# Kernel optimization log

Hardware: AMD Instinct MI355X
Metric: run time of the kernel (lower is better)

## Reference

```python
import jax, jax.numpy as jnp
import numpy as np

VOXEL_SIZE = np.array([0.1, 0.1, 0.1], np.float32)
PC_MIN = np.array([-70.4, -40.0, -3.0], np.float32)
STRIDE = 8
NZ, NY, NX = 5, 100, 176          # dense voxel grid dims at this stride (z, y, x)
G = 6                             # ROI grid size
C_IN, C_MID = 64, 32              # backbone channels, per-point MLP widths
N_ROIS, N_VOX = 256, 30000
FC = 256

_o = np.arange(-1, 2)
OFFSETS = np.stack(np.meshgrid(_o, _o, _o, indexing='ij'), -1).reshape(-1, 3).astype(np.int32)  # (27,3) (dx,dy,dz)


def setup_inputs() -> dict:
    rng = np.random.default_rng(0)
    # rois: [x, y, z, dx, dy, dz, heading]
    ctr = np.stack([rng.uniform(-60, 60, N_ROIS), rng.uniform(-35, 35, N_ROIS), rng.uniform(-2.0, 0.5, N_ROIS)], -1)
    size = np.stack([rng.uniform(3.0, 5.0, N_ROIS), rng.uniform(1.5, 2.2, N_ROIS), rng.uniform(1.3, 1.9, N_ROIS)], -1)
    yaw = rng.uniform(-np.pi, np.pi, (N_ROIS, 1))
    rois = np.concatenate([ctr, size, yaw], -1).astype(np.float32)
    # unique sparse voxel coords stored as (x, y, z)
    flat = rng.choice(NZ * NY * NX, N_VOX, replace=False)
    z, y, x = np.unravel_index(flat, (NZ, NY, NX))
    voxel_coords = np.stack([x, y, z], -1).astype(np.int32)

    def W(*s):
        return jnp.asarray((rng.standard_normal(s) / np.sqrt(s[-1])).astype(np.float32))

    pre = G ** 3 * C_MID  # 6912, channel-major flattened pooled features
    return dict(
        rois=jnp.asarray(rois),
        voxel_features=jnp.asarray(rng.standard_normal((N_VOX, C_IN)).astype(np.float32)),
        voxel_coords=jnp.asarray(voxel_coords),
        w_mlp1=W(C_IN, C_MID), w_mlp2=W(C_MID, C_MID),
        w_fc1=W(FC, pre), w_fc2=W(FC, FC),
        w_cls1=W(FC, FC), w_cls2=W(FC, FC), w_cls3=W(1, FC), b_cls3=jnp.zeros((1,), jnp.float32),
        w_iou1=W(FC, FC), w_iou2=W(FC, FC), w_iou3=W(1, FC), b_iou3=jnp.zeros((1,), jnp.float32),
        w_reg1=W(FC, FC), w_reg2=W(FC, FC), w_reg3=W(7, FC) * 0.001, b_reg3=jnp.zeros((7,), jnp.float32),
    )


def _grid_points(rois):
    # dense GxGxG grid in each roi local frame, rotated by heading, shifted to center
    idx = jnp.stack(jnp.meshgrid(*([jnp.arange(G)] * 3), indexing='ij'), -1).reshape(-1, 3).astype(jnp.float32)
    size = rois[:, 3:6]                                               # (N,3)
    local = (idx[None] + 0.5) / G * size[:, None] - size[:, None] * 0.5  # (N,216,3)
    c, s = jnp.cos(rois[:, 6])[:, None], jnp.sin(rois[:, 6])[:, None]
    gx = local[..., 0] * c - local[..., 1] * s
    gy = local[..., 0] * s + local[..., 1] * c
    pts = jnp.stack([gx, gy, local[..., 2]], -1) + rois[:, None, 0:3]
    return pts.reshape(-1, 3)                                         # (N*G^3, 3)


def _build_v2p(voxel_coords, n_vox):
    v2p = jnp.full((NZ, NY, NX), -1, jnp.int32)
    return v2p.at[voxel_coords[:, 2], voxel_coords[:, 1], voxel_coords[:, 0]].set(
        jnp.arange(n_vox, dtype=jnp.int32))


def _forward(rois, voxel_features, v2p, w_mlp1, w_mlp2, w_fc1, w_fc2,
             w_cls1, w_cls2, w_cls3, b_cls3, w_iou1, w_iou2, w_iou3, b_iou3,
             w_reg1, w_reg2, w_reg3, b_reg3):
    xyz = _grid_points(rois)                                          # (M,3)
    coords = (jnp.floor((xyz - jnp.asarray(PC_MIN)) / jnp.asarray(VOXEL_SIZE)).astype(jnp.int32)) // STRIDE
    nc = coords[:, None, :] + jnp.asarray(OFFSETS)[None]              # (M,27,3) (x,y,z)
    lim = jnp.array([NX, NY, NZ], jnp.int32)
    valid = jnp.all((nc >= 0) & (nc < lim), axis=-1)
    ncl = jnp.clip(nc, 0, lim - 1)
    vidx = v2p[ncl[..., 2], ncl[..., 1], ncl[..., 0]]                 # (M,27) voxel index or -1
    valid = valid & (vidx >= 0)
    feat = voxel_features[jnp.clip(vidx, 0)]                          # (M,27,C_IN) irregular gather
    h = jax.nn.relu(feat @ w_mlp1)
    h = jax.nn.relu(h @ w_mlp2)                                       # (M,27,C_MID)
    pooled = jnp.max(jnp.where(valid[..., None], h, 0.0), axis=1)     # max-pool over neighbors
    n = rois.shape[0]
    # torch: (N, G^3, C) -> permute(0,2,1) -> view(N, C*G^3, 1): channel-major flatten
    flat = pooled.reshape(n, G ** 3, C_MID).transpose(0, 2, 1).reshape(n, -1)
    x = jax.nn.relu(flat @ w_fc1.T)
    x = jax.nn.relu(x @ w_fc2.T)

    def head(h1, h2, h3, b3):
        y = jax.nn.relu(x @ h1.T)
        y = jax.nn.relu(y @ h2.T)
        return y @ h3.T + b3

    rcnn_cls = head(w_cls1, w_cls2, w_cls3, b_cls3)   # (N,1)
    rcnn_iou = head(w_iou1, w_iou2, w_iou3, b_iou3)   # (N,1)
    rcnn_reg = head(w_reg1, w_reg2, w_reg3, b_reg3)   # (N,7)
    return rcnn_cls, rcnn_iou, rcnn_reg


def reference(rois, voxel_features, voxel_coords, w_mlp1, w_mlp2, w_fc1, w_fc2,
              w_cls1, w_cls2, w_cls3, b_cls3, w_iou1, w_iou2, w_iou3, b_iou3,
              w_reg1, w_reg2, w_reg3, b_reg3):
    v2p = _build_v2p(voxel_coords, voxel_features.shape[0])
    return _forward(rois, voxel_features, v2p, w_mlp1, w_mlp2, w_fc1, w_fc2,
                    w_cls1, w_cls2, w_cls3, b_cls3, w_iou1, w_iou2, w_iou3, b_iou3,
                    w_reg1, w_reg2, w_reg3, b_reg3)
```

## Files before the change

### kernel.cpp

```cpp
#include <hip/hip_runtime.h>

#define NZD 5
#define NYD 100
#define NXD 176
#define NVOX 30000
#define NROI 256
#define CIN 64
#define CMID 32
#define GPTS 216
#define KDIM 6912
#define PBLK 18
#define SPLITK 27


__global__ __launch_bounds__(256) void k_scatter(const int* __restrict__ vc, int* __restrict__ v2p){
    int i = blockIdx.x*256 + threadIdx.x;
    if (i >= NVOX) return;
    int x = vc[i*3+0], y = vc[i*3+1], z = vc[i*3+2];
    v2p[(z*NYD + y)*NXD + x] = i;
}

__global__ __launch_bounds__(256) void k_vmlp(const float* __restrict__ feat,
                                              const float* __restrict__ w1,
                                              const float* __restrict__ w2,
                                              float* __restrict__ h){
    __shared__ float W1[CIN*CMID];
    __shared__ float W2[CMID*CMID];
    int t = threadIdx.x;
    for (int i = t; i < CIN*CMID; i += 256) W1[i] = w1[i];
    for (int i = t; i < CMID*CMID; i += 256) W2[i] = w2[i];
    __syncthreads();
    int v = blockIdx.x*256 + t;
    if (v >= NVOX) return;
    float h1[CMID];
    #pragma unroll
    for (int c = 0; c < CMID; ++c) h1[c] = 0.f;
    const float4* f4 = (const float4*)(feat + (size_t)v*CIN);
    #pragma unroll 4
    for (int k4 = 0; k4 < CIN/4; ++k4){
        float4 fv = f4[k4];
        int kb = k4*4;
        #pragma unroll
        for (int c = 0; c < CMID; ++c){
            h1[c] = fmaf(fv.x, W1[(kb+0)*CMID + c], h1[c]);
            h1[c] = fmaf(fv.y, W1[(kb+1)*CMID + c], h1[c]);
            h1[c] = fmaf(fv.z, W1[(kb+2)*CMID + c], h1[c]);
            h1[c] = fmaf(fv.w, W1[(kb+3)*CMID + c], h1[c]);
        }
    }
    #pragma unroll
    for (int c = 0; c < CMID; ++c) h1[c] = fmaxf(h1[c], 0.f);
    float h2[CMID];
    #pragma unroll
    for (int c = 0; c < CMID; ++c) h2[c] = 0.f;
    #pragma unroll 4
    for (int k = 0; k < CMID; ++k){
        float hv = h1[k];
        #pragma unroll
        for (int c = 0; c < CMID; ++c)
            h2[c] = fmaf(hv, W2[k*CMID + c], h2[c]);
    }
    float4* o4 = (float4*)(h + (size_t)v*CMID);
    #pragma unroll
    for (int q = 0; q < CMID/4; ++q)
        o4[q] = make_float4(fmaxf(h2[q*4+0],0.f), fmaxf(h2[q*4+1],0.f),
                            fmaxf(h2[q*4+2],0.f), fmaxf(h2[q*4+3],0.f));
}

__global__ __launch_bounds__(256) void k_pool(const float* __restrict__ rois,
                                              const int* __restrict__ v2p,
                                              const float* __restrict__ h,
                                              float* __restrict__ flat){
    __shared__ float P[PBLK*33];
    int r = blockIdx.y;
    int pbase = blockIdx.x * PBLK;
    int t = threadIdx.x;
    int g = t >> 5, lane = t & 31;
    float cx0 = rois[r*7+0], cy0 = rois[r*7+1], cz0 = rois[r*7+2];
    float dx  = rois[r*7+3], dy  = rois[r*7+4], dz  = rois[r*7+5];
    float yaw = rois[r*7+6];
    float cs = (float)cos((double)yaw);
    float sn = (float)sin((double)yaw);
    for (int pl = g; pl < PBLK; pl += 8){
        int p = pbase + pl;
        int i = p/36, j = (p/6)%6, k = p%6;
        int cX, cY, cZ;
        {
            #pragma clang fp contract(off)
            float lx = (((float)i + 0.5f)/6.0f)*dx - dx*0.5f;
            float ly = (((float)j + 0.5f)/6.0f)*dy - dy*0.5f;
            float lz = (((float)k + 0.5f)/6.0f)*dz - dz*0.5f;
            float gx = (lx*cs - ly*sn) + cx0;
            float gy = (lx*sn + ly*cs) + cy0;
            float gz = lz + cz0;
            float tx = (gx - (-70.4f)) / 0.1f;
            float ty = (gy - (-40.0f)) / 0.1f;
            float tz = (gz - (-3.0f))  / 0.1f;
            cX = ((int)floorf(tx)) >> 3;
            cY = ((int)floorf(ty)) >> 3;
            cZ = ((int)floorf(tz)) >> 3;
        }
        int vi[27];
        #pragma unroll
        for (int o = 0; o < 27; ++o){
            int ox = o % 3 - 1, oy = (o/3) % 3 - 1, oz = o/9 - 1;
            int nxc = cX+ox, nyc = cY+oy, nzc = cZ+oz;
            bool inb = ((unsigned)nxc < NXD) & ((unsigned)nyc < NYD) & ((unsigned)nzc < NZD);
            int cell = inb ? (nzc*NYD + nyc)*NXD + nxc : 0;
            int v = v2p[cell];
            vi[o] = inb ? v : -1;
        }
        float best = 0.f;
        #pragma unroll
        for (int o = 0; o < 27; ++o){
            int vc = vi[o] < 0 ? 0 : vi[o];
            float val = h[(size_t)vc*CMID + lane];
            best = fmaxf(best, vi[o] >= 0 ? val : 0.f);
        }
        P[pl*33 + lane] = best;
    }
    __syncthreads();
    for (int i2 = t; i2 < PBLK*CMID; i2 += 256){
        int pp = i2 % PBLK;
        int cc = i2 / PBLK;
        flat[(size_t)r*KDIM + cc*GPTS + pbase + pp] = P[pp*33 + cc];
    }
}

__global__ __launch_bounds__(256) void k_fc1(const float* __restrict__ A,
                                             const float* __restrict__ B,
                                             float* __restrict__ P){
    __shared__ float As[32][68];
    __shared__ float Bs[64][68];
    int t = threadIdx.x;
    int nb = blockIdx.x*64, mb = blockIdx.y*32, k0 = blockIdx.z*256;
    int tx = t & 15, ty = t >> 4;
    int lrow = t >> 4;
    int lcol = (t & 15)*4;
    float acc[2][4];
    #pragma unroll
    for (int i = 0; i < 2; ++i)
        #pragma unroll
        for (int j = 0; j < 4; ++j) acc[i][j] = 0.f;
    for (int kk = 0; kk < 4; ++kk){
        int ko = k0 + kk*64;
        #pragma unroll
        for (int it = 0; it < 2; ++it){
            int row = lrow + it*16;
            *(float4*)&As[row][lcol] = *(const float4*)&A[(size_t)(mb+row)*KDIM + ko + lcol];
        }
        #pragma unroll
        for (int it = 0; it < 4; ++it){
            int row = lrow + it*16;
            *(float4*)&Bs[row][lcol] = *(const float4*)&B[(size_t)(nb+row)*KDIM + ko + lcol];
        }
        __syncthreads();
        #pragma unroll 4
        for (int k4 = 0; k4 < 64; k4 += 4){
            float4 av[2], bv[4];
            #pragma unroll
            for (int i = 0; i < 2; ++i) av[i] = *(const float4*)&As[ty + 16*i][k4];
            #pragma unroll
            for (int j = 0; j < 4; ++j) bv[j] = *(const float4*)&Bs[tx + 16*j][k4];
            #pragma unroll
            for (int i = 0; i < 2; ++i)
                #pragma unroll
                for (int j = 0; j < 4; ++j){
                    acc[i][j] = fmaf(av[i].x, bv[j].x, acc[i][j]);
                    acc[i][j] = fmaf(av[i].y, bv[j].y, acc[i][j]);
                    acc[i][j] = fmaf(av[i].z, bv[j].z, acc[i][j]);
                    acc[i][j] = fmaf(av[i].w, bv[j].w, acc[i][j]);
                }
        }
        __syncthreads();
    }
    float* Pz = P + (size_t)blockIdx.z*65536;
    #pragma unroll
    for (int i = 0; i < 2; ++i)
        #pragma unroll
        for (int j = 0; j < 4; ++j)
            Pz[(size_t)(mb + ty + 16*i)*256 + nb + tx + 16*j] = acc[i][j];
}

__global__ __launch_bounds__(256) void k_red(const float* __restrict__ P,
                                             float* __restrict__ x1){
    int i = blockIdx.x*256 + threadIdx.x;
    float s = 0.f;
    #pragma unroll
    for (int z = 0; z < SPLITK; ++z) s += P[(size_t)z*65536 + i];
    x1[i] = s;
}

__global__ __launch_bounds__(256) void k_tgemm(
    const float* __restrict__ A0, long strideA, int reluA,
    const float* __restrict__ Wa, const float* __restrict__ Wb, const float* __restrict__ Wc,
    float* __restrict__ C0, long strideC)
{
    int z = blockIdx.z;
    const float* A = A0 + (size_t)z*strideA;
    const float* W = (z == 0) ? Wa : (z == 1) ? Wb : Wc;
    float* C = C0 + (size_t)z*strideC;
    __shared__ float As[32][68];
    __shared__ float Ws[32][68];
    int t = threadIdx.x;
    int nb = blockIdx.x*32, mb = blockIdx.y*32;
    int ty = t >> 4, tx = t & 15;
    float acc[2][2] = {{0.f,0.f},{0.f,0.f}};
    for (int kt = 0; kt < 4; ++kt){
        int ko = kt*64;
        #pragma unroll
        for (int it = 0; it < 2; ++it){
            int u = t + it*256;
            int row = u >> 4;
            int c4 = (u & 15) * 4;
            float4 av = *(const float4*)&A[(size_t)(mb+row)*256 + ko + c4];
            if (reluA){ av.x=fmaxf(av.x,0.f); av.y=fmaxf(av.y,0.f);
                        av.z=fmaxf(av.z,0.f); av.w=fmaxf(av.w,0.f); }
            *(float4*)&As[row][c4] = av;
            *(float4*)&Ws[row][c4] = *(const float4*)&W[(size_t)(nb+row)*256 + ko + c4];
        }
        __syncthreads();
        #pragma unroll
        for (int k4 = 0; k4 < 16; ++k4){
            float4 a0 = *(const float4*)&As[2*ty  ][k4*4];
            float4 a1 = *(const float4*)&As[2*ty+1][k4*4];
            float4 w0 = *(const float4*)&Ws[2*tx  ][k4*4];
            float4 w1 = *(const float4*)&Ws[2*tx+1][k4*4];
            acc[0][0]=fmaf(a0.x,w0.x,acc[0][0]); acc[0][0]=fmaf(a0.y,w0.y,acc[0][0]);
            acc[0][0]=fmaf(a0.z,w0.z,acc[0][0]); acc[0][0]=fmaf(a0.w,w0.w,acc[0][0]);
            acc[0][1]=fmaf(a0.x,w1.x,acc[0][1]); acc[0][1]=fmaf(a0.y,w1.y,acc[0][1]);
            acc[0][1]=fmaf(a0.z,w1.z,acc[0][1]); acc[0][1]=fmaf(a0.w,w1.w,acc[0][1]);
            acc[1][0]=fmaf(a1.x,w0.x,acc[1][0]); acc[1][0]=fmaf(a1.y,w0.y,acc[1][0]);
            acc[1][0]=fmaf(a1.z,w0.z,acc[1][0]); acc[1][0]=fmaf(a1.w,w0.w,acc[1][0]);
            acc[1][1]=fmaf(a1.x,w1.x,acc[1][1]); acc[1][1]=fmaf(a1.y,w1.y,acc[1][1]);
            acc[1][1]=fmaf(a1.z,w1.z,acc[1][1]); acc[1][1]=fmaf(a1.w,w1.w,acc[1][1]);
        }
        __syncthreads();
    }
    #pragma unroll
    for (int i = 0; i < 2; ++i)
        #pragma unroll
        for (int j = 0; j < 2; ++j)
            C[(size_t)(mb+2*ty+i)*256 + nb+2*tx+j] = fmaxf(acc[i][j], 0.f);
}

__global__ __launch_bounds__(256) void k_final(const float* __restrict__ y2,
    const float* __restrict__ wc3, const float* __restrict__ bc3,
    const float* __restrict__ wi3, const float* __restrict__ bi3,
    const float* __restrict__ wr3, const float* __restrict__ br3,
    float* __restrict__ out){
    __shared__ float red[4];
    int r = blockIdx.x, t = threadIdx.x;
    auto reduce_out = [&](float v, float bias, int idx){
        #pragma unroll
        for (int off = 32; off > 0; off >>= 1) v += __shfl_down(v, off);
        if ((t & 63) == 0) red[t >> 6] = v;
        __syncthreads();
        if (t == 0) out[idx] = red[0] + red[1] + red[2] + red[3] + bias;
        __syncthreads();
    };
    float yc = y2[(size_t)r*256 + t];
    float yi = y2[65536 + (size_t)r*256 + t];
    float yr = y2[131072 + (size_t)r*256 + t];
    reduce_out(yc*wc3[t], bc3[0], r);
    reduce_out(yi*wi3[t], bi3[0], 256 + r);
    for (int q = 0; q < 7; ++q)
        reduce_out(yr*wr3[q*256 + t], br3[q], 512 + r*7 + q);
}

extern "C" void kernel_launch(void* const* d_in, const int* in_sizes, int n_in,
                              void* d_out, int out_size, void* d_ws, size_t ws_size,
                              hipStream_t stream){
    const float* rois  = (const float*)d_in[0];
    const float* vfeat = (const float*)d_in[1];
    const int*   vcrd  = (const int*)d_in[2];
    const float* wm1   = (const float*)d_in[3];
    const float* wm2   = (const float*)d_in[4];
    const float* wfc1  = (const float*)d_in[5];
    const float* wfc2  = (const float*)d_in[6];
    const float* wc1   = (const float*)d_in[7];
    const float* wc2   = (const float*)d_in[8];
    const float* wc3   = (const float*)d_in[9];
    const float* bc3   = (const float*)d_in[10];
    const float* wi1   = (const float*)d_in[11];
    const float* wi2   = (const float*)d_in[12];
    const float* wi3   = (const float*)d_in[13];
    const float* bi3   = (const float*)d_in[14];
    const float* wr1   = (const float*)d_in[15];
    const float* wr2   = (const float*)d_in[16];
    const float* wr3   = (const float*)d_in[17];
    const float* br3   = (const float*)d_in[18];
    float* out = (float*)d_out;

    char* ws = (char*)d_ws;
    int*   v2p   = (int*)(ws + 0);
    float* h     = (float*)(ws + 352256);
    float* flat  = (float*)(ws + 4192512);
    float* x1    = (float*)(ws + 11270656);
    float* x2    = (float*)(ws + 11532800);
    float* y1    = (float*)(ws + 11794944);
    float* y2    = (float*)(ws + 12581376);
    float* parts = (float*)(ws + 13367808);

    k_scatter<<<dim3(118),      dim3(256), 0, stream>>>(vcrd, v2p);
    k_vmlp   <<<dim3(118),      dim3(256), 0, stream>>>(vfeat, wm1, wm2, h);
    k_pool   <<<dim3(12, 256),  dim3(256), 0, stream>>>(rois, v2p, h, flat);
    k_fc1    <<<dim3(4,8,SPLITK), dim3(256), 0, stream>>>(flat, wfc1, parts);
    k_red    <<<dim3(256),      dim3(256), 0, stream>>>(parts, x1);
    k_tgemm  <<<dim3(8,8,1),    dim3(256), 0, stream>>>(x1, 0,     1, wfc2, wfc2, wfc2, x2, 0);
    k_tgemm  <<<dim3(8,8,3),    dim3(256), 0, stream>>>(x2, 0,     0, wc1,  wi1,  wr1,  y1, 65536);
    k_tgemm  <<<dim3(8,8,3),    dim3(256), 0, stream>>>(y1, 65536, 0, wc2,  wi2,  wr2,  y2, 65536);
    k_final  <<<dim3(256),      dim3(256), 0, stream>>>(y2, wc3, bc3, wi3, bi3, wr3, br3, out);
}
```

Before: 208.9 us.

## Run fc1 split-K GEMM on bf16 MFMA with bf16 pooled features and weights

```diff
diff --git a/kernel.cpp b/kernel.cpp
--- a/kernel.cpp
+++ b/kernel.cpp
@@ -11,6 +11,14 @@
 #define KDIM 6912
 #define PBLK 18
 #define SPLITK 27
+
+typedef __attribute__((ext_vector_type(8))) short short8v;
+typedef __attribute__((ext_vector_type(4))) float f32x4;
+
+__device__ __forceinline__ unsigned short f2bf(float f){
+    unsigned int u = __float_as_uint(f);
+    return (unsigned short)((u + 0x7FFFu + ((u >> 16) & 1u)) >> 16);
+}
 
 
 __global__ __launch_bounds__(256) void k_scatter(const int* __restrict__ vc, int* __restrict__ v2p){
@@ -67,10 +75,20 @@
                             fmaxf(h2[q*4+2],0.f), fmaxf(h2[q*4+3],0.f));
 }
 
+__global__ __launch_bounds__(256) void k_cvt(const float* __restrict__ w,
+                                             unsigned short* __restrict__ o){
+    int i = (blockIdx.x*256 + threadIdx.x)*8;
+    float4 v0 = *(const float4*)&w[i];
+    float4 v1 = *(const float4*)&w[i+4];
+    unsigned short r[8] = { f2bf(v0.x), f2bf(v0.y), f2bf(v0.z), f2bf(v0.w),
+                            f2bf(v1.x), f2bf(v1.y), f2bf(v1.z), f2bf(v1.w) };
+    *(float4*)&o[i] = *(float4*)r;
+}
+
 __global__ __launch_bounds__(256) void k_pool(const float* __restrict__ rois,
                                               const int* __restrict__ v2p,
                                               const float* __restrict__ h,
-                                              float* __restrict__ flat){
+                                              unsigned short* __restrict__ flat){
     __shared__ float P[PBLK*33];
     int r = blockIdx.y;
     int pbase = blockIdx.x * PBLK;
@@ -123,63 +141,53 @@
     for (int i2 = t; i2 < PBLK*CMID; i2 += 256){
         int pp = i2 % PBLK;
         int cc = i2 / PBLK;
-        flat[(size_t)r*KDIM + cc*GPTS + pbase + pp] = P[pp*33 + cc];
-    }
-}
-
-__global__ __launch_bounds__(256) void k_fc1(const float* __restrict__ A,
-                                             const float* __restrict__ B,
-                                             float* __restrict__ P){
-    __shared__ float As[32][68];
-    __shared__ float Bs[64][68];
+        flat[(size_t)r*KDIM + cc*GPTS + pbase + pp] = f2bf(P[pp*33 + cc]);
+    }
+}
+
+__global__ __launch_bounds__(256) void k_fc1m(const unsigned short* __restrict__ A,
+                                              const unsigned short* __restrict__ B,
+                                              float* __restrict__ P){
+    __shared__ unsigned short As[64][136];
+    __shared__ unsigned short Bs[64][136];
     int t = threadIdx.x;
-    int nb = blockIdx.x*64, mb = blockIdx.y*32, k0 = blockIdx.z*256;
-    int tx = t & 15, ty = t >> 4;
-    int lrow = t >> 4;
-    int lcol = (t & 15)*4;
-    float acc[2][4];
-    #pragma unroll
-    for (int i = 0; i < 2; ++i)
-        #pragma unroll
-        for (int j = 0; j < 4; ++j) acc[i][j] = 0.f;
-    for (int kk = 0; kk < 4; ++kk){
-        int ko = k0 + kk*64;
-        #pragma unroll
-        for (int it = 0; it < 2; ++it){
-            int row = lrow + it*16;
-            *(float4*)&As[row][lcol] = *(const float4*)&A[(size_t)(mb+row)*KDIM + ko + lcol];
-        }
+    int nb = blockIdx.x*64, mb = blockIdx.y*64, k0 = blockIdx.z*256;
+    int wid = t >> 6, lane = t & 63;
+    int mo = (wid >> 1)*32, no = (wid & 1)*32;
+    f32x4 acc[2][2] = {};
+    for (int kr = 0; kr < 2; ++kr){
+        int ko = k0 + kr*128;
         #pragma unroll
         for (int it = 0; it < 4; ++it){
-            int row = lrow + it*16;
-            *(float4*)&Bs[row][lcol] = *(const float4*)&B[(size_t)(nb+row)*KDIM + ko + lcol];
-        }
-        __syncthreads();
-        #pragma unroll 4
-        for (int k4 = 0; k4 < 64; k4 += 4){
-            float4 av[2], bv[4];
+            int row = (t >> 4) + it*16;
+            int c8 = (t & 15)*8;
+            *(float4*)&As[row][c8] = *(const float4*)&A[(size_t)(mb+row)*KDIM + ko + c8];
+            *(float4*)&Bs[row][c8] = *(const float4*)&B[(size_t)(nb+row)*KDIM + ko + c8];
+        }
+        __syncthreads();
+        #pragma unroll
+        for (int ks = 0; ks < 4; ++ks){
+            int kc = ks*32 + (lane >> 4)*8;
+            short8v a0 = *(const short8v*)&As[mo      + (lane & 15)][kc];
+            short8v a1 = *(const short8v*)&As[mo + 16 + (lane & 15)][kc];
+            short8v b0 = *(const short8v*)&Bs[no      + (lane & 15)][kc];
+            short8v b1 = *(const short8v*)&Bs[no + 16 + (lane & 15)][kc];
+            acc[0][0] = __builtin_amdgcn_mfma_f32_16x16x32_bf16(a0, b0, acc[0][0], 0, 0, 0);
+            acc[0][1] = __builtin_amdgcn_mfma_f32_16x16x32_bf16(a0, b1, acc[0][1], 0, 0, 0);
+            acc[1][0] = __builtin_amdgcn_mfma_f32_16x16x32_bf16(a1, b0, acc[1][0], 0, 0, 0);
+            acc[1][1] = __builtin_amdgcn_mfma_f32_16x16x32_bf16(a1, b1, acc[1][1], 0, 0, 0);
+        }
+        __syncthreads();
+    }
+    float* Pz = P + (size_t)blockIdx.z*65536;
+    int crow = (lane >> 4)*4, ccol = lane & 15;
+    #pragma unroll
+    for (int s = 0; s < 2; ++s)
+        #pragma unroll
+        for (int u = 0; u < 2; ++u)
             #pragma unroll
-            for (int i = 0; i < 2; ++i) av[i] = *(const float4*)&As[ty + 16*i][k4];
-            #pragma unroll
-            for (int j = 0; j < 4; ++j) bv[j] = *(const float4*)&Bs[tx + 16*j][k4];
-            #pragma unroll
-            for (int i = 0; i < 2; ++i)
-                #pragma unroll
-                for (int j = 0; j < 4; ++j){
-                    acc[i][j] = fmaf(av[i].x, bv[j].x, acc[i][j]);
-                    acc[i][j] = fmaf(av[i].y, bv[j].y, acc[i][j]);
-                    acc[i][j] = fmaf(av[i].z, bv[j].z, acc[i][j]);
-                    acc[i][j] = fmaf(av[i].w, bv[j].w, acc[i][j]);
-                }
-        }
-        __syncthreads();
-    }
-    float* Pz = P + (size_t)blockIdx.z*65536;
-    #pragma unroll
-    for (int i = 0; i < 2; ++i)
-        #pragma unroll
-        for (int j = 0; j < 4; ++j)
-            Pz[(size_t)(mb + ty + 16*i)*256 + nb + tx + 16*j] = acc[i][j];
+            for (int r = 0; r < 4; ++r)
+                Pz[(size_t)(mb + mo + s*16 + crow + r)*256 + nb + no + u*16 + ccol] = acc[s][u][r];
 }
 
 __global__ __launch_bounds__(256) void k_red(const float* __restrict__ P,
@@ -293,22 +301,24 @@
     float* out = (float*)d_out;
 
     char* ws = (char*)d_ws;
-    int*   v2p   = (int*)(ws + 0);
-    float* h     = (float*)(ws + 352256);
-    float* flat  = (float*)(ws + 4192512);
-    float* x1    = (float*)(ws + 11270656);
-    float* x2    = (float*)(ws + 11532800);
-    float* y1    = (float*)(ws + 11794944);
-    float* y2    = (float*)(ws + 12581376);
-    float* parts = (float*)(ws + 13367808);
-
-    k_scatter<<<dim3(118),      dim3(256), 0, stream>>>(vcrd, v2p);
-    k_vmlp   <<<dim3(118),      dim3(256), 0, stream>>>(vfeat, wm1, wm2, h);
-    k_pool   <<<dim3(12, 256),  dim3(256), 0, stream>>>(rois, v2p, h, flat);
-    k_fc1    <<<dim3(4,8,SPLITK), dim3(256), 0, stream>>>(flat, wfc1, parts);
-    k_red    <<<dim3(256),      dim3(256), 0, stream>>>(parts, x1);
-    k_tgemm  <<<dim3(8,8,1),    dim3(256), 0, stream>>>(x1, 0,     1, wfc2, wfc2, wfc2, x2, 0);
-    k_tgemm  <<<dim3(8,8,3),    dim3(256), 0, stream>>>(x2, 0,     0, wc1,  wi1,  wr1,  y1, 65536);
-    k_tgemm  <<<dim3(8,8,3),    dim3(256), 0, stream>>>(y1, 65536, 0, wc2,  wi2,  wr2,  y2, 65536);
-    k_final  <<<dim3(256),      dim3(256), 0, stream>>>(y2, wc3, bc3, wi3, bi3, wr3, br3, out);
-}
+    int*            v2p   = (int*)(ws + 0);
+    float*          h     = (float*)(ws + 352256);
+    unsigned short* flat  = (unsigned short*)(ws + 4192512);
+    unsigned short* wb    = (unsigned short*)(ws + 7731456);
+    float*          parts = (float*)(ws + 11270656);
+    float*          x1    = (float*)(ws + 18348544);
+    float*          x2    = (float*)(ws + 18610688);
+    float*          y1    = (float*)(ws + 18872832);
+    float*          y2    = (float*)(ws + 19659264);
+
+    k_scatter<<<dim3(118),        dim3(256), 0, stream>>>(vcrd, v2p);
+    k_vmlp   <<<dim3(118),        dim3(256), 0, stream>>>(vfeat, wm1, wm2, h);
+    k_cvt    <<<dim3(864),        dim3(256), 0, stream>>>(wfc1, wb);
+    k_pool   <<<dim3(12, 256),    dim3(256), 0, stream>>>(rois, v2p, h, flat);
+    k_fc1m   <<<dim3(4,4,SPLITK), dim3(256), 0, stream>>>(flat, wb, parts);
+    k_red    <<<dim3(256),        dim3(256), 0, stream>>>(parts, x1);
+    k_tgemm  <<<dim3(8,8,1),      dim3(256), 0, stream>>>(x1, 0,     1, wfc2, wfc2, wfc2, x2, 0);
+    k_tgemm  <<<dim3(8,8,3),      dim3(256), 0, stream>>>(x2, 0,     0, wc1,  wi1,  wr1,  y1, 65536);
+    k_tgemm  <<<dim3(8,8,3),      dim3(256), 0, stream>>>(y1, 65536, 0, wc2,  wi2,  wr2,  y2, 65536);
+    k_final  <<<dim3(256),        dim3(256), 0, stream>>>(y2, wc3, bc3, wi3, bi3, wr3, br3, out);
+}
```

After: 193.3 us. -7.5%, faster.
